# Optimization experiments

Hardware: AMD Instinct MI355X
Metric: run time of the kernel (lower is better)

Reference implementation:

```python
import jax, jax.numpy as jnp
import numpy as np

B_GRAPHS = 16
N_PER_GRAPH = 128
N_NODES = B_GRAPHS * N_PER_GRAPH  # 2048
HIDDEN = 256
N_HEADS = 8
HEAD_DIM = HIDDEN // N_HEADS
N_LAYERS = 4
K_RPE = 4
N_EDGES = 32768
NUM_NODE_FEATS = 32
NUM_EDGE_TYPES = 16
MAX_DEGREE = 100
MLP_HID = HIDDEN // 2


def _layernorm(x, s, b):
    m = x.mean(-1, keepdims=True)
    v = jnp.var(x, axis=-1, keepdims=True)
    return (x - m) / jnp.sqrt(v + 1e-5) * s + b


def setup_inputs() -> dict:
    key = jax.random.key(0)
    ks = jax.random.split(key, 24)
    s = 0.02
    x_idx = jax.random.randint(ks[0], (N_NODES,), 0, NUM_NODE_FEATS)
    # edges are intra-graph (the torch code drops cross-graph edges)
    src = jax.random.randint(ks[1], (N_EDGES,), 0, N_NODES)
    dst = (src // N_PER_GRAPH) * N_PER_GRAPH + jax.random.randint(ks[2], (N_EDGES,), 0, N_PER_GRAPH)
    edge_index = jnp.stack([src, dst])
    edge_attr = jax.random.randint(ks[3], (N_EDGES,), 0, NUM_EDGE_TYPES)
    batch = jnp.repeat(jnp.arange(B_GRAPHS), N_PER_GRAPH)
    L = N_LAYERS
    return {
        'x_idx': x_idx, 'edge_index': edge_index, 'edge_attr': edge_attr, 'batch': batch,
        'node_emb': jax.random.normal(ks[4], (NUM_NODE_FEATS, HIDDEN)) * s,
        'edge_emb': jax.random.normal(ks[5], (NUM_EDGE_TYPES, N_HEADS)) * s,
        'degree_emb': jax.random.normal(ks[6], (MAX_DEGREE + 1, HIDDEN)) * s,
        'rpe_W1': jax.random.normal(ks[7], (K_RPE + 1, MLP_HID)) * s,
        'rpe_b1': jnp.zeros((MLP_HID,)),
        'rpe_W2': jax.random.normal(ks[8], (MLP_HID, N_HEADS)) * s,
        'rpe_b2': jnp.zeros((N_HEADS,)),
        'Wq': jax.random.normal(ks[9], (L, HIDDEN, HIDDEN)) * s, 'bq': jnp.zeros((L, HIDDEN)),
        'Wk': jax.random.normal(ks[10], (L, HIDDEN, HIDDEN)) * s, 'bk': jnp.zeros((L, HIDDEN)),
        'Wv': jax.random.normal(ks[11], (L, HIDDEN, HIDDEN)) * s, 'bv': jnp.zeros((L, HIDDEN)),
        'Wo': jax.random.normal(ks[12], (L, HIDDEN, HIDDEN)) * s, 'bo': jnp.zeros((L, HIDDEN)),
        'ln1_s': jnp.ones((L, HIDDEN)), 'ln1_b': jnp.zeros((L, HIDDEN)),
        'ln2_s': jnp.ones((L, HIDDEN)), 'ln2_b': jnp.zeros((L, HIDDEN)),
        'ff_W1': jax.random.normal(ks[13], (L, HIDDEN, 2 * HIDDEN)) * s, 'ff_b1': jnp.zeros((L, 2 * HIDDEN)),
        'ff_W2': jax.random.normal(ks[14], (L, 2 * HIDDEN, HIDDEN)) * s, 'ff_b2': jnp.zeros((L, HIDDEN)),
    }


def _forward(x_idx, edge_index, edge_attr, batch,
             node_emb, edge_emb, degree_emb, rpe_W1, rpe_b1, rpe_W2, rpe_b2,
             Wq, bq, Wk, bk, Wv, bv, Wo, bo, ln1_s, ln1_b, ln2_s, ln2_b,
             ff_W1, ff_b1, ff_W2, ff_b2):
    B, n, H, N = B_GRAPHS, N_PER_GRAPH, N_HEADS, N_NODES
    x = node_emb[x_idx]                               # [N, d]
    src, dst = edge_index[0], edge_index[1]
    # degrees from source endpoints (scatter_add in torch)
    deg = jnp.zeros((N,), jnp.int32).at[src].add(1)
    deg_c = jnp.minimum(deg, MAX_DEGREE)

    # ---- RRWP + edge-type attention bias, block-diagonal over graphs ----
    g = batch[src]
    intra = (batch[src] == batch[dst])                # torch code skips cross-graph edges
    u = src % n
    v = dst % n
    intra_f = intra.astype(jnp.float32)
    inv_du = intra_f / jnp.maximum(deg[src], 1).astype(jnp.float32)
    inv_dv = intra_f / jnp.maximum(deg[dst], 1).astype(jnp.float32)
    # random-walk transition matrix per graph [B, n, n]
    T = (jnp.zeros((B, n, n), jnp.float32)
         .at[g, u, v].add(inv_du)
         .at[g, v, u].add(inv_dv))
    # symmetric edge-type bias per graph [B, n, n, H]
    ev = edge_emb[edge_attr] * intra_f[:, None]
    EB = (jnp.zeros((B, n, n, H), jnp.float32)
          .at[g, u, v].add(ev)
          .at[g, v, u].add(ev))
    # walk powers I, T, T^2, ..., T^K -> [B, n, n, K+1]
    I = jnp.broadcast_to(jnp.eye(n, dtype=jnp.float32), (B, n, n))
    powers = [I, T]
    cur = T
    for _ in range(2, K_RPE + 1):
        cur = cur @ T
        powers.append(cur)
    walk = jnp.stack(powers, axis=-1)
    pair = jax.nn.relu(walk @ rpe_W1 + rpe_b1) @ rpe_W2 + rpe_b2   # [B, n, n, H]
    block = (pair + EB).transpose(0, 3, 1, 2)                      # [B, H, n, n]
    ib = jnp.arange(B)
    full = jnp.full((H, B, n, B, n), -jnp.inf, jnp.float32)
    full = full.at[:, ib, :, ib, :].set(block)                     # diag blocks
    attn_bias = full.reshape(H, N, N)

    # ---- transformer stack ----
    deg_vec = degree_emb[deg_c]
    scale = 1.0 / jnp.sqrt(jnp.float32(HEAD_DIM))
    for l in range(N_LAYERS):
        x = x + deg_vec
        Q = (x @ Wq[l] + bq[l]).reshape(N, H, HEAD_DIM)
        K_ = (x @ Wk[l] + bk[l]).reshape(N, H, HEAD_DIM)
        V = (x @ Wv[l] + bv[l]).reshape(N, H, HEAD_DIM)
        scores = jnp.einsum('ihd,jhd->hij', Q, K_) * scale + attn_bias
        aw = jax.nn.softmax(scores, axis=-1)
        out = jnp.einsum('hij,jhd->ihd', aw, V).reshape(N, HIDDEN)
        out = out @ Wo[l] + bo[l]
        x = _layernorm(x + out, ln1_s[l], ln1_b[l])
        ff = jax.nn.relu(x @ ff_W1[l] + ff_b1[l]) @ ff_W2[l] + ff_b2[l]
        x = _layernorm(x + ff, ln2_s[l], ln2_b[l])
    # global add pool
    return jax.ops.segment_sum(x, batch, num_segments=B)


def reference(x_idx, edge_index, edge_attr, batch,
              node_emb, edge_emb, degree_emb, rpe_W1, rpe_b1, rpe_W2, rpe_b2,
              Wq, bq, Wk, bk, Wv, bv, Wo, bo, ln1_s, ln1_b, ln2_s, ln2_b,
              ff_W1, ff_b1, ff_W2, ff_b2):
    return _forward(x_idx, edge_index, edge_attr, batch,
                    node_emb, edge_emb, degree_emb, rpe_W1, rpe_b1, rpe_W2, rpe_b2,
                    Wq, bq, Wk, bk, Wv, bv, Wo, bo, ln1_s, ln1_b, ln2_s, ln2_b,
                    ff_W1, ff_b1, ff_W2, ff_b2)
```

## Files before the change

### kernel.cpp

```cpp
#include <hip/hip_runtime.h>
#include <hip/hip_bf16.h>

#define B_GRAPHS 16
#define NPG 128
#define NN 2048
#define HIDDEN 256
#define N_HEADS 8
#define HEAD_DIM 32
#define N_LAYERS 4
#define N_EDGES 32768
#define MLP_HID 128
#define MAX_DEG 100

typedef __hip_bfloat16 bf16;
typedef unsigned short ushort_t;
typedef __attribute__((ext_vector_type(8))) short short8;
typedef __attribute__((ext_vector_type(4))) float f32x4;

__device__ __forceinline__ float us2f(ushort_t u) {
    return __uint_as_float(((unsigned)u) << 16);
}
__device__ __forceinline__ ushort_t f2us(float f) {
    unsigned u = __float_as_uint(f);
    return (ushort_t)((u + 0x7FFFu + ((u >> 16) & 1u)) >> 16);
}
__device__ __forceinline__ bool is_bf16_mode(const unsigned* probe) {
    return probe[0] != 0x3F800000u;
}
#define MFMA16(a, b, c) __builtin_amdgcn_mfma_f32_16x16x32_bf16(a, b, c, 0, 0, 0)

__device__ __forceinline__ void gload_lds16(const void* g, void* l) {
    __builtin_amdgcn_global_load_lds(
        (const __attribute__((address_space(1))) unsigned int*)g,
        (__attribute__((address_space(3))) unsigned int*)l, 16, 0, 0);
}
#define SBAR __builtin_amdgcn_s_barrier()
#define WAITP8 asm volatile("s_waitcnt vmcnt(8) lgkmcnt(0)" ::: "memory")
#define WAITLAST asm volatile("s_waitcnt vmcnt(0) lgkmcnt(0)" ::: "memory")
#define LBAR do { asm volatile("s_waitcnt lgkmcnt(0)" ::: "memory"); SBAR; \
                  asm volatile("" ::: "memory"); } while (0)

#define NW 23
__device__ const int c_wsizes[NW] = {
    8192, 128, 25856, 640, 128, 1024, 8,
    262144, 1024, 262144, 1024, 262144, 1024, 262144, 1024,
    1024, 1024, 1024, 1024,
    524288, 2048, 524288, 1024};
#define TOTW 2144392

#define OFF_NODE_EMB 0
#define OFF_EDGE_EMB 8192
#define OFF_DEG_EMB  8320
#define OFF_RPE_W1   34176
#define OFF_RPE_B1   34816
#define OFF_RPE_W2   34944
#define OFF_RPE_B2   35968
#define OFF_BO       1087624
#define OFF_LN1S     1088648
#define OFF_LN1B     1089672
#define OFF_LN2S     1090696
#define OFF_LN2B     1091720
#define OFF_FFB1     1617032
#define OFF_FFB2     2143368

#define WB_QKV 0
#define WB_O   786432
#define WB_F1  1048576
#define WB_F2  1572864
#define WB_TOT 2097152
#define QKVB_TOT 3072

#define ZERO_BLKS 2310
#define CONV_BLKS 8389
#define TP_BLKS   2048

struct SrcPtrs { const void* p[NW]; };

__global__ __launch_bounds__(256) void prep1(SrcPtrs sp, const unsigned* __restrict__ probe,
                                             float* __restrict__ Wc, float* __restrict__ qkvb,
                                             f32x4* __restrict__ zerop,
                                             ushort_t* __restrict__ WB) {
    __shared__ float tile[32][33];
    int b = blockIdx.x;
    bool isbf = is_bf16_mode(probe);
    auto rd = [&](int seg, int off) -> float {
        return isbf ? us2f(((const ushort_t*)sp.p[seg])[off])
                    : ((const float*)sp.p[seg])[off];
    };
    if (b < ZERO_BLKS) {
        f32x4 z;
        z[0] = 0.f; z[1] = 0.f; z[2] = 0.f; z[3] = 0.f;
        zerop[b * 256 + threadIdx.x] = z;
    } else if (b < ZERO_BLKS + CONV_BLKS) {
        int i = (b - ZERO_BLKS) * 256 + threadIdx.x;
        if (i < TOTW) {
            int seg = 0, off = i;
            while (seg < NW - 1 && off >= c_wsizes[seg]) { off -= c_wsizes[seg]; seg++; }
            bool dead = (seg == 7 || seg == 9 || seg == 11 || seg == 13 ||
                         seg == 19 || seg == 21);
            if (!dead) Wc[i] = rd(seg, off);
        } else if (i < TOTW + QKVB_TOT) {
            int j = i - TOTW;
            int l = j / 768, n = j % 768, which = n >> 8, nn = n & 255;
            int seg = (which == 0) ? 8 : (which == 1) ? 10 : 12;
            qkvb[j] = rd(seg, l * 256 + nn);
        }
    } else {
        int tb = b - ZERO_BLKS - CONV_BLKS;
        int seg, soff, srcN, k0, n0, dK;
        size_t doff;
        if (tb < 768) {
            int mat = tb >> 6, t = tb & 63;
            int l = mat / 3, which = mat % 3;
            seg = 7 + which * 2;
            soff = l * 65536; srcN = 256;
            k0 = (t >> 3) * 32; n0 = (t & 7) * 32;
            doff = (size_t)l * 196608 + (size_t)which * 65536; dK = 256;
        } else if (tb < 1024) {
            int u = tb - 768, l = u >> 6, t = u & 63;
            seg = 13; soff = l * 65536; srcN = 256;
            k0 = (t >> 3) * 32; n0 = (t & 7) * 32;
            doff = WB_O + (size_t)l * 65536; dK = 256;
        } else if (tb < 1536) {
            int u = tb - 1024, l = u >> 7, t = u & 127;
            seg = 19; soff = l * 131072; srcN = 512;
            k0 = (t >> 4) * 32; n0 = (t & 15) * 32;
            doff = WB_F1 + (size_t)l * 131072; dK = 256;
        } else {
            int u = tb - 1536, l = u >> 7, t = u & 127;
            seg = 21; soff = l * 131072; srcN = 256;
            k0 = (t >> 3) * 32; n0 = (t & 7) * 32;
            doff = WB_F2 + (size_t)l * 131072; dK = 512;
        }
        int xcol = threadIdx.x & 31, y8 = threadIdx.x >> 5;
        const void* srcp = sp.p[seg];
#pragma unroll
        for (int rr = 0; rr < 4; rr++) {
            int row = y8 * 4 + rr;
            int off = soff + (k0 + row) * srcN + n0 + xcol;
            tile[row][xcol] = isbf ? us2f(((const ushort_t*)srcp)[off])
                                   : ((const float*)srcp)[off];
        }
        __syncthreads();
#pragma unroll
        for (int rr = 0; rr < 4; rr++) {
            int nrow = y8 * 4 + rr;
            WB[doff + (size_t)(n0 + nrow) * dK + k0 + xcol] = f2us(tile[xcol][nrow]);
        }
    }
}

__global__ void deg_kernel(const int* __restrict__ src, int* __restrict__ deg) {
    int e = blockIdx.x * blockDim.x + threadIdx.x;
    if (e < N_EDGES) atomicAdd(&deg[src[e]], 1);
}

__global__ void prep2(const int* __restrict__ xidx, const int* __restrict__ deg,
                      const float* __restrict__ emb, const float* __restrict__ demb,
                      float* __restrict__ x, ushort_t* __restrict__ xb,
                      const int* __restrict__ ei, const int* __restrict__ eattr,
                      const int* __restrict__ batch, const float* __restrict__ edge_emb,
                      float* __restrict__ T, float* __restrict__ bias) {
    int b = blockIdx.x;
    if (b < 2048) {
        int i = b * 256 + threadIdx.x;
        int node = i >> 8, c = i & 255;
        float v = emb[xidx[node] * HIDDEN + c] + demb[min(deg[node], MAX_DEG) * HIDDEN + c];
        x[i] = v;
        xb[i] = f2us(v);
    } else {
        int idx = (b - 2048) * 256 + threadIdx.x;
        int e = idx >> 3, h = idx & 7;
        int s = ei[e], d = ei[N_EDGES + e];
        if (batch[s] != batch[d]) return;
        int g = batch[s];
        int u = s & (NPG - 1), v = d & (NPG - 1);
        if (h == 0) {
            atomicAdd(&T[(g * NPG + u) * NPG + v], 1.0f / (float)max(deg[s], 1));
            atomicAdd(&T[(g * NPG + v) * NPG + u], 1.0f / (float)max(deg[d], 1));
        }
        float ev = edge_emb[eattr[e] * N_HEADS + h];
        atomicAdd(&bias[(((size_t)(g * N_HEADS + h) * NPG + u) * NPG + v)], ev);
        atomicAdd(&bias[(((size_t)(g * N_HEADS + h) * NPG + v) * NPG + u)], ev);
    }
}

__global__ void matmul128(const float* __restrict__ A, const float* __restrict__ B,
                          float* __restrict__ C) {
    int g = blockIdx.x / NPG;
    int row = blockIdx.x % NPG;
    int col = threadIdx.x;
    const float* Ag = A + (size_t)g * NPG * NPG;
    const float* Bg = B + (size_t)g * NPG * NPG;
    __shared__ float arow[NPG];
    arow[col] = Ag[row * NPG + col];
    __syncthreads();
    float acc = 0.f;
#pragma unroll 8
    for (int k = 0; k < NPG; k++) acc += arow[k] * Bg[k * NPG + col];
    C[((size_t)g * NPG + row) * NPG + col] = acc;
}

__global__ void matmul128_dual(const float* __restrict__ T2, const float* __restrict__ T,
                               float* __restrict__ T3, float* __restrict__ T4) {
    int half = blockIdx.x >> 11;
    int bid = blockIdx.x & 2047;
    int g = bid / NPG, row = bid % NPG, col = threadIdx.x;
    const float* Ag = T2 + (size_t)g * NPG * NPG;
    const float* Bg = (half ? T2 : T) + (size_t)g * NPG * NPG;
    float* Cg = (half ? T4 : T3) + (size_t)g * NPG * NPG;
    __shared__ float arow[NPG];
    arow[col] = Ag[row * NPG + col];
    __syncthreads();
    float acc = 0.f;
#pragma unroll 8
    for (int k = 0; k < NPG; k++) acc += arow[k] * Bg[k * NPG + col];
    Cg[row * NPG + col] = acc;
}

__global__ __launch_bounds__(256) void rpe_kernel(
    const float* __restrict__ T, const float* __restrict__ T2,
    const float* __restrict__ T3, const float* __restrict__ T4,
    const float* __restrict__ W1, const float* __restrict__ b1,
    const float* __restrict__ W2, const float* __restrict__ b2,
    float* __restrict__ bias) {
    __shared__ float sW1[5][MLP_HID];
    __shared__ float sb1[MLP_HID];
    __shared__ float sW2[MLP_HID][N_HEADS];
    int t = threadIdx.x;
    for (int i = t; i < 5 * MLP_HID; i += 256) sW1[i / MLP_HID][i % MLP_HID] = W1[i];
    for (int i = t; i < MLP_HID; i += 256) sb1[i] = b1[i];
    for (int i = t; i < MLP_HID * N_HEADS; i += 256) sW2[i / N_HEADS][i % N_HEADS] = W2[i];
    __syncthreads();
    int p = blockIdx.x * 256 + t;
    int g = p / (NPG * NPG);
    int rem = p % (NPG * NPG);
    int i = rem / NPG, j = rem % NPG;
    float f0 = (i == j) ? 1.f : 0.f;
    float f1 = T[p], f2 = T2[p], f3 = T3[p], f4 = T4[p];
    float acc[N_HEADS];
#pragma unroll
    for (int h = 0; h < N_HEADS; h++) acc[h] = b2[h];
#pragma unroll 4
    for (int m = 0; m < MLP_HID; m++) {
        float hv = sb1[m] + f0 * sW1[0][m] + f1 * sW1[1][m] + f2 * sW1[2][m] +
                   f3 * sW1[3][m] + f4 * sW1[4][m];
        hv = fmaxf(hv, 0.f);
#pragma unroll
        for (int h = 0; h < N_HEADS; h++) acc[h] += hv * sW2[m][h];
    }
#pragma unroll
    for (int h = 0; h < N_HEADS; h++)
        bias[(((size_t)(g * N_HEADS + h) * NPG + i) * NPG + j)] += acc[h];
}

__global__ __launch_bounds__(512, 1) void qkv_attn(
    const ushort_t* __restrict__ x_bf, const ushort_t* __restrict__ WT,
    const float* __restrict__ qb, const float* __restrict__ bias,
    ushort_t* __restrict__ ao) {
    int g = blockIdx.x >> 3, h = blockIdx.x & 7;
    int o = threadIdx.x >> 6, lane = threadIdx.x & 63;
    int lr = lane & 15, lq = lane >> 4;

    __shared__ char Wbuf[3][16384];
    __shared__ ushort_t Ks[NPG][40];
    __shared__ ushort_t VT[32][136];
    __shared__ ushort_t P[8][16][136];

    const ushort_t* xg = x_bf + (size_t)g * NPG * HIDDEN;
    int row16 = o * 16;

    short8 Ax[8];
#pragma unroll
    for (int kk = 0; kk < 8; kk++)
        Ax[kk] = *(const short8*)(xg + (size_t)(row16 + lr) * 256 + kk * 32 + lq * 8);
    float bqv[2], bkv[2], bvv[2];
#pragma unroll
    for (int j = 0; j < 2; j++) {
        int c = h * 32 + j * 16 + lr;
        bqv[j] = qb[c]; bkv[j] = qb[256 + c]; bvv[j] = qb[512 + c];
    }
    asm volatile("s_waitcnt vmcnt(0) lgkmcnt(0)" ::: "memory");

    auto stageW = [&](int rowbase, int c) {
        const char* gW = (const char*)WT;
        char* lb = &Wbuf[c][0] + o * 2048;
#pragma unroll
        for (int it = 0; it < 2; it++) {
            int j = o * 2048 + it * 1024 + lane * 16;
            int n = j >> 9, off = j & 511;
            gload_lds16(gW + (size_t)(rowbase + n) * 512 + (off ^ ((n & 7) << 4)),
                        lb + it * 1024);
        }
        __builtin_amdgcn_sched_barrier(0);
    };
    stageW(h * 32, 0);
    stageW(256 + h * 32, 1);
    stageW(512 + h * 32, 2);

    const float* bg = bias + (size_t)(g * N_HEADS + h) * NPG * NPG;
    float bgv[8][4];
#pragma unroll
    for (int r = 0; r < 4; r++) {
        int i = row16 + lq * 4 + r;
#pragma unroll
        for (int jt = 0; jt < 8; jt++)
            bgv[jt][r] = bg[(size_t)i * NPG + jt * 16 + lr];
    }
    __builtin_amdgcn_sched_barrier(0);

    auto rdW = [&](int c, int jt, int kk) -> short8 {
        int n = jt * 16 + lr;
        int off = n * 512 + ((kk * 64 + lq * 16) ^ ((n & 7) << 4));
        return *(const short8*)(&Wbuf[c][off]);
    };

    f32x4 qa[2]{}, ka[2]{}, va[2]{};
    asm volatile("s_waitcnt vmcnt(36)" ::: "memory"); SBAR;
#pragma unroll
    for (int kk = 0; kk < 8; kk++)
#pragma unroll
        for (int j = 0; j < 2; j++)
            qa[j] = MFMA16(Ax[kk], rdW(0, j, kk), qa[j]);

    asm volatile("s_waitcnt vmcnt(34)" ::: "memory"); SBAR;
#pragma unroll
    for (int kk = 0; kk < 8; kk++)
#pragma unroll
        for (int j = 0; j < 2; j++)
            ka[j] = MFMA16(Ax[kk], rdW(1, j, kk), ka[j]);

    asm volatile("s_waitcnt vmcnt(32)" ::: "memory"); SBAR;
#pragma unroll
    for (int kk = 0; kk < 8; kk++)
#pragma unroll
        for (int j = 0; j < 2; j++)
            va[j] = MFMA16(Ax[kk], rdW(2, j, kk), va[j]);

#pragma unroll
    for (int j = 0; j < 2; j++) {
        int c = j * 16 + lr;
#pragma unroll
        for (int r = 0; r < 4; r++) {
            int row = row16 + lq * 4 + r;
            P[o][lq * 4 + r][c] = f2us(qa[j][r] + bqv[j]);
            Ks[row][c] = f2us(ka[j][r] + bkv[j]);
            VT[c][row] = f2us(va[j][r] + bvv[j]);
        }
    }
    __syncthreads();

    short8 qf = *(const short8*)(&P[o][lr][lq * 8]);
    f32x4 S[8];
    f32x4 zero;
    zero[0] = 0.f; zero[1] = 0.f; zero[2] = 0.f; zero[3] = 0.f;
#pragma unroll
    for (int jt = 0; jt < 8; jt++) {
        short8 kf = *(const short8*)(&Ks[jt * 16 + lr][lq * 8]);
        S[jt] = MFMA16(qf, kf, zero);
    }

    const float scale = 0.17677669529663687f;
    float lrow[4];
#pragma unroll
    for (int r = 0; r < 4; r++) {
        float mx = -1e30f;
#pragma unroll
        for (int jt = 0; jt < 8; jt++) {
            float s = S[jt][r] * scale + bgv[jt][r];
            S[jt][r] = s;
            mx = fmaxf(mx, s);
        }
#pragma unroll
        for (int m = 1; m < 16; m <<= 1) mx = fmaxf(mx, __shfl_xor(mx, m));
        float sum = 0.f;
#pragma unroll
        for (int jt = 0; jt < 8; jt++) {
            float e = __expf(S[jt][r] - mx);
            S[jt][r] = e;
            sum += e;
        }
#pragma unroll
        for (int m = 1; m < 16; m <<= 1) sum += __shfl_xor(sum, m);
        lrow[r] = sum;
    }

#pragma unroll
    for (int jt = 0; jt < 8; jt++)
#pragma unroll
        for (int r = 0; r < 4; r++)
            P[o][lq * 4 + r][jt * 16 + lr] = f2us(S[jt][r]);

    f32x4 O[2]{};
#pragma unroll
    for (int k0 = 0; k0 < NPG; k0 += 32) {
        short8 pa = *(const short8*)(&P[o][lr][k0 + lq * 8]);
#pragma unroll
        for (int dt = 0; dt < 2; dt++) {
            short8 vb = *(const short8*)(&VT[dt * 16 + lr][k0 + lq * 8]);
            O[dt] = MFMA16(pa, vb, O[dt]);
        }
    }
#pragma unroll
    for (int r = 0; r < 4; r++) {
        float inv = 1.f / lrow[r];
        int row = g * NPG + row16 + lq * 4 + r;
#pragma unroll
        for (int dt = 0; dt < 2; dt++)
            ao[(size_t)row * HIDDEN + h * 32 + dt * 16 + lr] = f2us(O[dt][r] * inv);
    }
}

__global__ __launch_bounds__(512, 2) void fused_mlp(
    const ushort_t* __restrict__ ao, const ushort_t* __restrict__ WoT,
    const float* __restrict__ bo, const float* __restrict__ ln1s,
    const float* __restrict__ ln1b,
    const ushort_t* __restrict__ F1T, const ushort_t* __restrict__ F2T,
    const float* __restrict__ fb1, const float* __restrict__ fb2,
    const float* __restrict__ ln2s, const float* __restrict__ ln2b,
    const float* __restrict__ xin, const int* __restrict__ deg,
    const float* __restrict__ demb, int add_deg,
    float* __restrict__ xout, ushort_t* __restrict__ xb,
    float* __restrict__ poolf, int do_pool) {
    int m0 = blockIdx.x * 8;
    int wave = threadIdx.x >> 6, lane = threadIdx.x & 63;
    int lr = lane & 15, lq = lane >> 4;
    int ar = m0 + (lr & 7);

    __shared__ ushort_t Wbuf[2][32768];
    __shared__ ushort_t xs_bf[8][264];
    __shared__ ushort_t ffh[8][520];
    __shared__ float ws[8][16], qs[8][16];

    auto stageO = [&](int h, int b) {
        const char* gW = (const char*)WoT;
        char* lb = (char*)&Wbuf[b][0] + wave * 8192;
#pragma unroll
        for (int it = 0; it < 8; it++) {
            int j = wave * 8192 + it * 1024 + lane * 16;
            int n = j >> 8, off = j & 255;
            gload_lds16(gW + n * 512 + h * 256 + (off ^ ((n & 7) << 4)), lb + it * 1024);
        }
        __builtin_amdgcn_sched_barrier(0);
    };
    auto stageF1 = [&](int q, int b) {
        const char* gW = (const char*)F1T;
        char* lb = (char*)&Wbuf[b][0] + wave * 8192;
#pragma unroll
        for (int it = 0; it < 8; it++) {
            int j = wave * 8192 + it * 1024 + lane * 16;
            int n = j >> 9, off = j & 511;
            gload_lds16(gW + (q * 128 + n) * 512 + (off ^ ((n & 7) << 4)), lb + it * 1024);
        }
        __builtin_amdgcn_sched_barrier(0);
    };
    auto stageF2 = [&](int q, int b) {
        const char* gW = (const char*)F2T;
        char* lb = (char*)&Wbuf[b][0] + wave * 8192;
#pragma unroll
        for (int it = 0; it < 8; it++) {
            int j = wave * 8192 + it * 1024 + lane * 16;
            int n = j >> 8, off = j & 255;
            gload_lds16(gW + n * 1024 + q * 256 + (off ^ ((n & 7) << 4)), lb + it * 1024);
        }
        __builtin_amdgcn_sched_barrier(0);
    };

    float bo_v[2], l1s[2], l1b[2], fb2v[2], l2s[2], l2b[2], xres[2][4], fb1q[4];
#pragma unroll
    for (int jt = 0; jt < 2; jt++) {
        int col = wave * 32 + jt * 16 + lr;
        bo_v[jt] = bo[col]; l1s[jt] = ln1s[col]; l1b[jt] = ln1b[col];
        fb2v[jt] = fb2[col]; l2s[jt] = ln2s[col]; l2b[jt] = ln2b[col];
#pragma unroll
        for (int r = 0; r < 4; r++) {
            int row = m0 + ((lq * 4 + r) & 7);
            xres[jt][r] = xin[(size_t)row * 256 + col];
        }
    }
#pragma unroll
    for (int q = 0; q < 4; q++) fb1q[q] = fb1[q * 128 + wave * 16 + lr];
    int dg4[4];
    if (add_deg) {
#pragma unroll
        for (int r = 0; r < 4; r++)
            dg4[r] = min(deg[m0 + ((lq * 4 + r) & 7)], MAX_DEG);
    }
    short8 Af[8];
#pragma unroll
    for (int t = 0; t < 8; t++)
        Af[t] = *(const short8*)(ao + (size_t)ar * 256 + t * 32 + lq * 8);

    stageO(0, 0);
    stageO(1, 1);

    f32x4 acc[2]{};
#pragma unroll
    for (int h = 0; h < 2; h++) {
        WAITP8; SBAR; asm volatile("" ::: "memory");
#pragma unroll
        for (int kk = 0; kk < 4; kk++) {
            short8 a = Af[h * 4 + kk];
#pragma unroll
            for (int jt = 0; jt < 2; jt++) {
                int n = wave * 32 + jt * 16 + lr;
                int bo_ = n * 256 + ((kk * 64 + lq * 16) ^ ((n & 7) << 4));
                short8 bf = *(const short8*)((const char*)&Wbuf[h][0] + bo_);
                acc[jt] = MFMA16(a, bf, acc[jt]);
            }
        }
        LBAR;
        if (h == 0) stageF1(0, 0);
        else        stageF1(1, 1);
    }

    float valLN[2][4], meanst[4];
#pragma unroll
    for (int r = 0; r < 4; r++) {
        float s = 0.f;
#pragma unroll
        for (int jt = 0; jt < 2; jt++) {
            float v = acc[jt][r] + bo_v[jt] + xres[jt][r];
            valLN[jt][r] = v;
            s += v;
        }
#pragma unroll
        for (int m = 1; m < 16; m <<= 1) s += __shfl_xor(s, m);
        if (lr == 0) ws[wave][lq * 4 + r] = s;
    }
    LBAR;
#pragma unroll
    for (int r = 0; r < 4; r++) {
        int rr = lq * 4 + r;
        float sum = 0.f;
#pragma unroll
        for (int c = 0; c < 8; c++) sum += ws[c][rr];
        float mean = sum * (1.f / 256.f);
        meanst[r] = mean;
        float q = 0.f;
#pragma unroll
        for (int jt = 0; jt < 2; jt++) {
            float d = valLN[jt][r] - mean;
            q += d * d;
        }
#pragma unroll
        for (int m = 1; m < 16; m <<= 1) q += __shfl_xor(q, m);
        if (lr == 0) qs[wave][rr] = q;
    }
    LBAR;
#pragma unroll
    for (int r = 0; r < 4; r++) {
        int rr = lq * 4 + r;
        float qsum = 0.f;
#pragma unroll
        for (int c = 0; c < 8; c++) qsum += qs[c][rr];
        float rstd = rsqrtf(qsum * (1.f / 256.f) + 1e-5f);
#pragma unroll
        for (int jt = 0; jt < 2; jt++) {
            int col = wave * 32 + jt * 16 + lr;
            float y = (valLN[jt][r] - meanst[r]) * rstd * l1s[jt] + l1b[jt];
            valLN[jt][r] = y;
            if (rr < 8) xs_bf[rr][col] = f2us(y);
        }
    }

#pragma unroll
    for (int q = 0; q < 4; q++) {
        WAITP8; SBAR; asm volatile("" ::: "memory");
        f32x4 a1{};
        int nl = wave * 16 + lr;
#pragma unroll
        for (int kk = 0; kk < 8; kk++) {
            short8 a = *(const short8*)(&xs_bf[lr & 7][kk * 32 + lq * 8]);
            int bo_ = nl * 512 + ((kk * 64 + lq * 16) ^ ((nl & 7) << 4));
            short8 bf = *(const short8*)((const char*)&Wbuf[q & 1][0] + bo_);
            a1 = MFMA16(a, bf, a1);
        }
        int col = q * 128 + wave * 16 + lr;
#pragma unroll
        for (int r = 0; r < 4; r++) {
            int rr = lq * 4 + r;
            if (rr < 8) ffh[rr][col] = f2us(fmaxf(a1[r] + fb1q[q], 0.f));
        }
        LBAR;
        if (q < 2) stageF1(q + 2, q & 1);
        else       stageF2(q - 2, q & 1);
    }

    f32x4 acc2[2]{};
#pragma unroll
    for (int q = 0; q < 4; q++) {
        if (q == 3) { WAITLAST; } else { WAITP8; }
        SBAR; asm volatile("" ::: "memory");
#pragma unroll
        for (int kk = 0; kk < 4; kk++) {
            short8 a = *(const short8*)(&ffh[lr & 7][q * 128 + kk * 32 + lq * 8]);
#pragma unroll
            for (int jt = 0; jt < 2; jt++) {
                int n = wave * 32 + jt * 16 + lr;
                int bo_ = n * 256 + ((kk * 64 + lq * 16) ^ ((n & 7) << 4));
                short8 bf = *(const short8*)((const char*)&Wbuf[q & 1][0] + bo_);
                acc2[jt] = MFMA16(a, bf, acc2[jt]);
            }
        }
        LBAR;
        if (q < 2) stageF2(q + 2, q & 1);
    }

    float val2[2][4];
#pragma unroll
    for (int r = 0; r < 4; r++) {
        int rr = lq * 4 + r;
        float s = 0.f;
#pragma unroll
        for (int jt = 0; jt < 2; jt++) {
            float v = acc2[jt][r] + fb2v[jt] + valLN[jt][r];
            val2[jt][r] = v;
            s += v;
        }
#pragma unroll
        for (int m = 1; m < 16; m <<= 1) s += __shfl_xor(s, m);
        if (lr == 0) ws[wave][rr] = s;
    }
    __syncthreads();
#pragma unroll
    for (int r = 0; r < 4; r++) {
        int rr = lq * 4 + r;
        float sum = 0.f;
#pragma unroll
        for (int c = 0; c < 8; c++) sum += ws[c][rr];
        float mean = sum * (1.f / 256.f);
        meanst[r] = mean;
        float q = 0.f;
#pragma unroll
        for (int jt = 0; jt < 2; jt++) {
            float d = val2[jt][r] - mean;
            q += d * d;
        }
#pragma unroll
        for (int m = 1; m < 16; m <<= 1) q += __shfl_xor(q, m);
        if (lr == 0) qs[wave][rr] = q;
    }
    __syncthreads();
    float psum[2] = {0.f, 0.f};
#pragma unroll
    for (int r = 0; r < 4; r++) {
        int rr = lq * 4 + r;
        float qsum = 0.f;
#pragma unroll
        for (int c = 0; c < 8; c++) qsum += qs[c][rr];
        float rstd = rsqrtf(qsum * (1.f / 256.f) + 1e-5f);
        if (rr < 8) {
            int row = m0 + rr;
#pragma unroll
            for (int jt = 0; jt < 2; jt++) {
                int col = wave * 32 + jt * 16 + lr;
                float y = (val2[jt][r] - meanst[r]) * rstd * l2s[jt] + l2b[jt];
                if (add_deg) y += demb[dg4[r] * 256 + col];
                xout[(size_t)row * 256 + col] = y;
                xb[(size_t)row * 256 + col] = f2us(y);
                if (do_pool) psum[jt] += y;
            }
        }
    }
    if (do_pool && lq < 2) {
        int g = m0 >> 7;
#pragma unroll
        for (int jt = 0; jt < 2; jt++) {
            int col = wave * 32 + jt * 16 + lr;
            atomicAdd(&poolf[g * 256 + col], psum[jt]);
        }
    }
}

__global__ void pool_kernel(const float* __restrict__ poolf, void* __restrict__ out,
                            const unsigned* __restrict__ probe) {
    int i = blockIdx.x * 256 + threadIdx.x;
    float acc = poolf[i];
    if (is_bf16_mode(probe))
        ((bf16*)out)[i] = __float2bfloat16(acc);
    else
        ((float*)out)[i] = acc;
}

extern "C" void kernel_launch(void* const* d_in, const int* in_sizes, int n_in,
                              void* d_out, int out_size, void* d_ws, size_t ws_size,
                              hipStream_t stream) {
    const int* x_idx      = (const int*)d_in[0];
    const int* edge_index = (const int*)d_in[1];
    const int* edge_attr  = (const int*)d_in[2];
    const int* batch      = (const int*)d_in[3];
    const unsigned* probe = (const unsigned*)d_in[19];

    char* base = (char*)d_ws;
    float* Wc    = (float*)base;       base += (size_t)TOTW * 4;
    float* x     = (float*)base;       base += (size_t)NN * HIDDEN * 4;
    float* T     = (float*)base;       base += 262144 * 4;
    float* bias  = (float*)base;       base += (size_t)2097152 * 4;
    int*   deg   = (int*)base;         base += 2048 * 4;
    float* poolf = (float*)base;       base += 4096 * 4;
    float* T2    = (float*)base;       base += 262144 * 4;
    float* T3    = (float*)base;       base += 262144 * 4;
    float* T4    = (float*)base;       base += 262144 * 4;
    float* qkvb  = (float*)base;       base += QKVB_TOT * 4;
    ushort_t* WB    = (ushort_t*)base; base += (size_t)WB_TOT * 2;
    ushort_t* x_bf  = (ushort_t*)base; base += (size_t)NN * HIDDEN * 2;
    ushort_t* ao_bf = (ushort_t*)base; base += (size_t)NN * HIDDEN * 2;

    SrcPtrs sp;
    for (int i = 0; i < NW; i++) sp.p[i] = d_in[4 + i];

    prep1<<<ZERO_BLKS + CONV_BLKS + TP_BLKS, 256, 0, stream>>>(sp, probe, Wc, qkvb,
                                                               (f32x4*)T, WB);
    deg_kernel<<<N_EDGES / 256, 256, 0, stream>>>(edge_index, deg);
    prep2<<<3072, 256, 0, stream>>>(x_idx, deg, Wc + OFF_NODE_EMB, Wc + OFF_DEG_EMB,
                                    x, x_bf, edge_index, edge_attr, batch,
                                    Wc + OFF_EDGE_EMB, T, bias);
    matmul128<<<B_GRAPHS * NPG, NPG, 0, stream>>>(T, T, T2);
    matmul128_dual<<<2 * B_GRAPHS * NPG, NPG, 0, stream>>>(T2, T, T3, T4);
    rpe_kernel<<<(B_GRAPHS * NPG * NPG) / 256, 256, 0, stream>>>(
        T, T2, T3, T4, Wc + OFF_RPE_W1, Wc + OFF_RPE_B1, Wc + OFF_RPE_W2, Wc + OFF_RPE_B2,
        bias);

    for (int l = 0; l < N_LAYERS; l++) {
        qkv_attn<<<B_GRAPHS * N_HEADS, 512, 0, stream>>>(
            x_bf, WB + WB_QKV + (size_t)l * 196608, qkvb + l * 768, bias, ao_bf);
        fused_mlp<<<NN / 8, 512, 0, stream>>>(
            ao_bf, WB + WB_O + (size_t)l * 65536, Wc + OFF_BO + l * 256,
            Wc + OFF_LN1S + l * 256, Wc + OFF_LN1B + l * 256,
            WB + WB_F1 + (size_t)l * 131072, WB + WB_F2 + (size_t)l * 131072,
            Wc + OFF_FFB1 + l * 512, Wc + OFF_FFB2 + l * 256,
            Wc + OFF_LN2S + l * 256, Wc + OFF_LN2B + l * 256, x,
            deg, Wc + OFF_DEG_EMB, (l < N_LAYERS - 1) ? 1 : 0, x, x_bf,
            poolf, (l == N_LAYERS - 1) ? 1 : 0);
    }
    pool_kernel<<<16, 256, 0, stream>>>(poolf, d_out, probe);
}
```

Before: 323.0 us.

## Rewrite RPE MLP kernel with bf16 MFMA for both layers

The RPE bias MLP used to run per pair in scalar fp32 FMAs over 128 hidden units and 8 heads. It is now two bf16 MFMA 16x16 matmuls per 16-pair tile, with the hidden activations staged in swizzled LDS. Each block handles one row i of one graph, and each wave handles 32 columns. This cuts the ALU cost of the RPE stage but rounds the inputs and weights to bf16, which lowers precision. The waves use only a waitcnt between the LDS write and read instead of a barrier, which is safe only because each wave uses its own LDS slice.

```diff
diff --git a/kernel.cpp b/kernel.cpp
--- a/kernel.cpp
+++ b/kernel.cpp
@@ -224,34 +224,90 @@
     const float* __restrict__ W1, const float* __restrict__ b1,
     const float* __restrict__ W2, const float* __restrict__ b2,
     float* __restrict__ bias) {
-    __shared__ float sW1[5][MLP_HID];
-    __shared__ float sb1[MLP_HID];
-    __shared__ float sW2[MLP_HID][N_HEADS];
-    int t = threadIdx.x;
-    for (int i = t; i < 5 * MLP_HID; i += 256) sW1[i / MLP_HID][i % MLP_HID] = W1[i];
-    for (int i = t; i < MLP_HID; i += 256) sb1[i] = b1[i];
-    for (int i = t; i < MLP_HID * N_HEADS; i += 256) sW2[i / N_HEADS][i % N_HEADS] = W2[i];
-    __syncthreads();
-    int p = blockIdx.x * 256 + t;
-    int g = p / (NPG * NPG);
-    int rem = p % (NPG * NPG);
-    int i = rem / NPG, j = rem % NPG;
-    float f0 = (i == j) ? 1.f : 0.f;
-    float f1 = T[p], f2 = T2[p], f3 = T3[p], f4 = T4[p];
-    float acc[N_HEADS];
-#pragma unroll
-    for (int h = 0; h < N_HEADS; h++) acc[h] = b2[h];
-#pragma unroll 4
-    for (int m = 0; m < MLP_HID; m++) {
-        float hv = sb1[m] + f0 * sW1[0][m] + f1 * sW1[1][m] + f2 * sW1[2][m] +
-                   f3 * sW1[3][m] + f4 * sW1[4][m];
-        hv = fmaxf(hv, 0.f);
-#pragma unroll
-        for (int h = 0; h < N_HEADS; h++) acc[h] += hv * sW2[m][h];
-    }
-#pragma unroll
-    for (int h = 0; h < N_HEADS; h++)
-        bias[(((size_t)(g * N_HEADS + h) * NPG + i) * NPG + j)] += acc[h];
+    int g = blockIdx.x >> 7, i = blockIdx.x & 127;
+    int w = threadIdx.x >> 6, lane = threadIdx.x & 63;
+    int lr = lane & 15, lq = lane >> 4;
+    __shared__ __align__(16) ushort_t hid[4][4096];
+
+    int pbase = (g * 128 + i) * 128;
+    int j0w = w * 32;
+
+    f32x4 zero;
+    zero[0] = 0.f; zero[1] = 0.f; zero[2] = 0.f; zero[3] = 0.f;
+
+    short8 b1f[8];
+#pragma unroll
+    for (int nt = 0; nt < 8; nt++) {
+        short8 v{};
+        if (lq == 0) {
+            int n = nt * 16 + lr;
+#pragma unroll
+            for (int e = 0; e < 5; e++) v[e] = (short)f2us(W1[e * 128 + n]);
+        }
+        b1f[nt] = v;
+    }
+    short8 b2f[4];
+#pragma unroll
+    for (int kt = 0; kt < 4; kt++) {
+        short8 v{};
+        if (lr < 8) {
+#pragma unroll
+            for (int e = 0; e < 8; e++)
+                v[e] = (short)f2us(W2[(kt * 32 + lq * 8 + e) * 8 + lr]);
+        }
+        b2f[kt] = v;
+    }
+    float b1v[8];
+#pragma unroll
+    for (int nt = 0; nt < 8; nt++) b1v[nt] = b1[nt * 16 + lr];
+    float b2v = (lr < 8) ? b2[lr] : 0.f;
+
+#pragma unroll
+    for (int mt = 0; mt < 2; mt++) {
+        int j0 = j0w + mt * 16;
+        short8 af{};
+        if (lq == 0) {
+            int p = pbase + j0 + lr;
+            af[0] = (short)f2us((i == j0 + lr) ? 1.f : 0.f);
+            af[1] = (short)f2us(T[p]);
+            af[2] = (short)f2us(T2[p]);
+            af[3] = (short)f2us(T3[p]);
+            af[4] = (short)f2us(T4[p]);
+        }
+        f32x4 h[8];
+#pragma unroll
+        for (int nt = 0; nt < 8; nt++) h[nt] = MFMA16(af, b1f[nt], zero);
+#pragma unroll
+        for (int nt = 0; nt < 8; nt++) {
+#pragma unroll
+            for (int r = 0; r < 4; r++) {
+                int row = mt * 16 + lq * 4 + r;
+                int colb = (nt * 32 + lr * 2) ^ ((row & 7) << 4);
+                *(ushort_t*)((char*)&hid[w][0] + row * 256 + colb) =
+                    f2us(fmaxf(h[nt][r] + b1v[nt], 0.f));
+            }
+        }
+    }
+    asm volatile("s_waitcnt lgkmcnt(0)" ::: "memory");
+
+#pragma unroll
+    for (int mt = 0; mt < 2; mt++) {
+        f32x4 o;
+        o[0] = 0.f; o[1] = 0.f; o[2] = 0.f; o[3] = 0.f;
+#pragma unroll
+        for (int kt = 0; kt < 4; kt++) {
+            int row = mt * 16 + lr;
+            int colb = (kt * 64 + lq * 16) ^ ((lr & 7) << 4);
+            short8 a = *(const short8*)((const char*)&hid[w][0] + row * 256 + colb);
+            o = MFMA16(a, b2f[kt], o);
+        }
+        if (lr < 8) {
+            size_t base2 = (((size_t)(g * N_HEADS + lr) * NPG + i) * NPG) + j0w + mt * 16;
+#pragma unroll
+            for (int r = 0; r < 4; r++)
+                bias[base2 + lq * 4 + r] += o[r] + b2v;
+        }
+    }
 }
 
 __global__ __launch_bounds__(512, 1) void qkv_attn(
@@ -718,7 +774,7 @@
                                     Wc + OFF_EDGE_EMB, T, bias);
     matmul128<<<B_GRAPHS * NPG, NPG, 0, stream>>>(T, T, T2);
     matmul128_dual<<<2 * B_GRAPHS * NPG, NPG, 0, stream>>>(T2, T, T3, T4);
-    rpe_kernel<<<(B_GRAPHS * NPG * NPG) / 256, 256, 0, stream>>>(
+    rpe_kernel<<<B_GRAPHS * NPG, 256, 0, stream>>>(
         T, T2, T3, T4, Wc + OFF_RPE_W1, Wc + OFF_RPE_B1, Wc + OFF_RPE_W2, Wc + OFF_RPE_B2,
         bias);
 
```

Result: no change. 320.7 us (-0.7%).
